# Optimization experiments

Hardware: AMD Instinct MI355X
Metric: run time of the kernel (lower is better)

Reference implementation:

```python
import jax, jax.numpy as jnp
import numpy as np

N = 10000          # nodes
E = 160000         # edges (avg degree 16)
H = 32             # hidden_dim
ND = 64            # node_dim
ED = 16            # edge_dim
MH = 128           # edge_mlp_hidden
MP_STEPS = 3


def setup_inputs() -> dict:
    key = jax.random.key(0)
    ks = jax.random.split(key, 10)
    s = lambda d: 1.0 / np.sqrt(d)
    return {
        "x": jax.random.normal(ks[0], (N, ND), jnp.float32),
        "edge_index": jax.random.randint(ks[1], (2, E), 0, N, dtype=jnp.int64),
        "edge_attr": jax.random.normal(ks[2], (E, ED), jnp.float32),
        # node_proj: Linear(node_dim -> hidden_dim)
        "Wp": jax.random.normal(ks[3], (ND, H), jnp.float32) * s(ND),
        "bp": jnp.zeros((H,), jnp.float32),
        # edge network MLP: edge_dim -> MH -> H*H
        "W1": jax.random.normal(ks[4], (ED, MH), jnp.float32) * s(ED),
        "b1": jnp.zeros((MH,), jnp.float32),
        "W2": jax.random.normal(ks[5], (MH, H * H), jnp.float32) * s(MH),
        "b2": jnp.zeros((H * H,), jnp.float32),
        # GRUCell params (torch layout: stacked [r, z, n], shape (3H, H))
        "w_ih": jax.random.normal(ks[6], (3 * H, H), jnp.float32) * s(H),
        "w_hh": jax.random.normal(ks[7], (3 * H, H), jnp.float32) * s(H),
        "b_ih": jnp.zeros((3 * H,), jnp.float32),
        "b_hh": jnp.zeros((3 * H,), jnp.float32),
    }


def gru_cell(x, h, w_ih, w_hh, b_ih, b_hh):
    # torch.nn.GRUCell semantics, gates stacked [r, z, n]
    gi = x @ w_ih.T + b_ih
    gh = h @ w_hh.T + b_hh
    i_r, i_z, i_n = jnp.split(gi, 3, axis=-1)
    h_r, h_z, h_n = jnp.split(gh, 3, axis=-1)
    r = jax.nn.sigmoid(i_r + h_r)
    z = jax.nn.sigmoid(i_z + h_z)
    n = jnp.tanh(i_n + r * h_n)
    return (1.0 - z) * n + z * h


def reference(x, edge_index, edge_attr, Wp, bp, W1, b1, W2, b2, w_ih, w_hh, b_ih, b_hh):
    h = x @ Wp + bp  # (N, H)
    # per-edge weight matrices; edge_attr is loop-invariant so compute once
    We = (jax.nn.relu(edge_attr @ W1 + b1) @ W2 + b2).reshape(E, H, H)
    src = edge_index[0]  # h_j (message source)
    dst = edge_index[1]  # aggregation target (PyG source_to_target flow)
    for _ in range(MP_STEPS):
        msg = jnp.einsum('eij,ej->ei', We, h[src])          # (E, H) per-edge GEMV
        agg = jax.ops.segment_sum(msg, dst, num_segments=N)  # scatter-add
        h = gru_cell(agg, h, w_ih, w_hh, b_ih, b_hh)
    return h
```

## Files before the change

### kernel.cpp

```cpp
#include <hip/hip_runtime.h>
#include <stdint.h>

#define H   32
#define ND  64
#define ED  16
#define MH  128
#define HH  1024

__device__ __forceinline__ float bf2f(uint16_t u) {
    union { uint32_t u; float f; } v; v.u = ((uint32_t)u) << 16; return v.f;
}
__device__ __forceinline__ uint16_t f2bf(float f) {
    union { float f; uint32_t u; } v; v.f = f;
    return (uint16_t)((v.u + 0x7FFFu + ((v.u >> 16) & 1u)) >> 16);
}
__device__ __forceinline__ float ldf(const void* p, size_t i, int isf32) {
    return isf32 ? ((const float*)p)[i] : bf2f(((const uint16_t*)p)[i]);
}

__global__ void k_detect(const uint16_t* __restrict__ xr,
                         const int* __restrict__ ei, int nedges,
                         int* __restrict__ flags) {
    __shared__ int s_bad, s_hi;
    int t = threadIdx.x;
    if (t == 0) { s_bad = 0; s_hi = 0; }
    __syncthreads();
    int bad = 0;
    for (int i = t; i < 2048; i += 256) {
        uint16_t u = xr[i];
        int e = (u >> 7) & 0xFF;
        if (!(u == 0 || (e >= 96 && e <= 144))) bad++;
    }
    atomicAdd(&s_bad, bad);
    int mm = nedges < 4096 ? nedges : 4096;
    int hi = 0;
    for (int i = t; i < mm; i += 256) hi |= (ei[2 * i + 1] != 0);
    if (hi) atomicOr(&s_hi, 1);
    __syncthreads();
    if (t == 0) {
        flags[0] = (s_bad > 204) ? 1 : 0;
        flags[1] = (s_hi == 0) ? 1 : 0;
    }
}

__device__ __forceinline__ int load_idx(const int* __restrict__ ei, int is64,
                                        long long pos, int nnodes) {
    int v = is64 ? (int)(((const long long*)ei)[pos]) : ei[pos];
    v = v < 0 ? 0 : v;
    return v >= nnodes ? nnodes - 1 : v;
}

__global__ void k_hist(const int* __restrict__ ei, const int* __restrict__ flags,
                       int* __restrict__ deg, int nedges, int nnodes) {
    int e = blockIdx.x * 256 + threadIdx.x;
    if (e >= nedges) return;
    int s = load_idx(ei, flags[1], e, nnodes);
    atomicAdd(&deg[s], 1);
}

__global__ void k_scan(const int* __restrict__ deg, int* __restrict__ cursor,
                       int nnodes) {
    __shared__ int tot[256];
    int t = threadIdx.x;
    int C = (nnodes + 255) >> 8;
    int b = t * C, e = b + C < nnodes ? b + C : nnodes;
    int s = 0;
    for (int i = b; i < e; i++) s += deg[i];
    tot[t] = s;
    __syncthreads();
    if (t == 0) {
        int acc = 0;
        for (int i = 0; i < 256; i++) { int v = tot[i]; tot[i] = acc; acc += v; }
    }
    __syncthreads();
    int acc = tot[t];
    for (int i = b; i < e; i++) { cursor[i] = acc; acc += deg[i]; }
}

__global__ void k_scatter(const int* __restrict__ ei, const int* __restrict__ flags,
                          int* __restrict__ cursor, int* __restrict__ perm,
                          int nedges, int nnodes) {
    int e = blockIdx.x * 256 + threadIdx.x;
    if (e >= nedges) return;
    int s = load_idx(ei, flags[1], e, nnodes);
    int p = atomicAdd(&cursor[s], 1);
    perm[p] = e;
}

__global__ __launch_bounds__(256) void k_node_proj(
    const void* __restrict__ x, const void* __restrict__ wp,
    const void* __restrict__ bp, float* __restrict__ h, int nnodes,
    const int* __restrict__ flags)
{
    __shared__ float wp_s[ND][H];
    __shared__ float x_s[8][ND + 1];
    int isf32 = flags[0];
    int t = threadIdx.x;
    for (int i = t; i < ND * H; i += 256) wp_s[i >> 5][i & 31] = ldf(wp, i, isf32);
    for (int i = t; i < 8 * ND; i += 256) {
        int row = i >> 6, col = i & 63;
        int gn = blockIdx.x * 8 + row;
        x_s[row][col] = (gn < nnodes) ? ldf(x, (size_t)gn * ND + col, isf32) : 0.f;
    }
    __syncthreads();
    int nl = t >> 5, c = t & 31;
    int n = blockIdx.x * 8 + nl;
    if (n >= nnodes) return;
    float acc = ldf(bp, c, isf32);
#pragma unroll
    for (int k = 0; k < ND; k++) acc += x_s[nl][k] * wp_s[k][c];
    h[(size_t)n * H + c] = acc;
}

__global__ void k_permw2(const void* __restrict__ w2g, float* __restrict__ Bp,
                         const int* __restrict__ flags) {
    int isf32 = flags[0];
    int idx = blockIdx.x * 256 + threadIdx.x;
    if (idx >= MH * HH) return;
    int k = idx / HH, col = idx % HH;
    int i = col >> 5, j = col & 31;
    Bp[(size_t)j * 4096 + i * 128 + k] = ldf(w2g, idx, isf32);
}

__global__ __launch_bounds__(256) void k_T4(
    const float* __restrict__ Bp, const float* __restrict__ h,
    float* __restrict__ Tall, int nnodes)
{
    __shared__ float h_s[64 * 32];
    int t = threadIdx.x;
    int cbq = blockIdx.x & 3;
    int n0 = (blockIdx.x >> 2) * 64;
    int c = cbq * 1024 + t * 4;

    for (int i = t; i < 64 * 32; i += 256) {
        int n = i >> 5;
        h_s[i] = (n0 + n < nnodes) ? h[(size_t)(n0 + n) * H + (i & 31)] : 0.f;
    }
    float4 Breg[32];
#pragma unroll
    for (int j = 0; j < 32; j++)
        Breg[j] = *((const float4*)&Bp[(size_t)j * 4096 + c]);
    __syncthreads();

    int nmax = nnodes - n0; if (nmax > 64) nmax = 64;
    int n = 0;
    for (; n + 2 <= nmax; n += 2) {
        float4 a0 = {0.f,0.f,0.f,0.f}, a1 = {0.f,0.f,0.f,0.f};
#pragma unroll
        for (int j = 0; j < 32; j++) {
            float h0 = h_s[n * 32 + j], h1 = h_s[(n + 1) * 32 + j];
            float4 b = Breg[j];
            a0.x += h0 * b.x; a0.y += h0 * b.y; a0.z += h0 * b.z; a0.w += h0 * b.w;
            a1.x += h1 * b.x; a1.y += h1 * b.y; a1.z += h1 * b.z; a1.w += h1 * b.w;
        }
        *((float4*)&Tall[(size_t)(n0 + n) * 4096 + c]) = a0;
        *((float4*)&Tall[(size_t)(n0 + n + 1) * 4096 + c]) = a1;
    }
    if (n < nmax) {
        float4 a0 = {0.f,0.f,0.f,0.f};
#pragma unroll
        for (int j = 0; j < 32; j++) {
            float h0 = h_s[n * 32 + j];
            float4 b = Breg[j];
            a0.x += h0 * b.x; a0.y += h0 * b.y; a0.z += h0 * b.z; a0.w += h0 * b.w;
        }
        *((float4*)&Tall[(size_t)(n0 + n) * 4096 + c]) = a0;
    }
}

__global__ __launch_bounds__(256) void k_u(
    const void* __restrict__ b2g, const float* __restrict__ h,
    float* __restrict__ u, int nnodes, const int* __restrict__ flags)
{
    __shared__ float b2_s[32 * 33];
    __shared__ float h_s[8 * 32];
    int isf32 = flags[0];
    int t = threadIdx.x;
    int n0 = blockIdx.x * 8;
    for (int idx = t; idx < 1024; idx += 256) {
        int i = idx >> 5, j = idx & 31;
        b2_s[i * 33 + j] = ldf(b2g, idx, isf32);
    }
    for (int i = t; i < 8 * 32; i += 256) {
        int n = i >> 5;
        h_s[i] = (n0 + n < nnodes) ? h[(size_t)(n0 + n) * H + (i & 31)] : 0.f;
    }
    __syncthreads();
    int nl = t >> 5, i = t & 31;
    if (n0 + nl >= nnodes) return;
    float acc = 0.f;
#pragma unroll
    for (int j = 0; j < 32; j++) acc += b2_s[i * 33 + j] * h_s[nl * 32 + j];
    u[(size_t)(n0 + nl) * 32 + i] = acc;
}

__global__ __launch_bounds__(256) void k_edge4(
    const void* __restrict__ ea, const void* __restrict__ w1,
    const void* __restrict__ b1g, const float* __restrict__ Tall,
    const float* __restrict__ u, const int* __restrict__ ei,
    const int* __restrict__ perm, const int* __restrict__ degp,
    const int* __restrict__ rendp, const int* __restrict__ flags,
    float* __restrict__ agg, int nedges, int nnodes)
{
    int n = blockIdx.x;
    int dcount = degp[n];
    if (dcount == 0) return;
    int rstart = rendp[n] - dcount;

    __shared__ float T_lds[32 * 132];
    __shared__ float hid_s[16 * 132];
    __shared__ float w1_s[ED * MH];
    __shared__ float ea_f[16 * ED];
    __shared__ float b1_s[MH];
    __shared__ float u_lds[32];
    __shared__ int   e_s[16], d_s[16];

    int t = threadIdx.x;
    int isf32 = flags[0], is64 = flags[1];

    for (int f = t; f < 1024; f += 256) {
        float4 q = *((const float4*)&Tall[(size_t)n * 4096 + f * 4]);
        int i = f >> 5, k4 = (f & 31) * 4;
        *((float4*)&T_lds[i * 132 + k4]) = q;
    }
    for (int i = t; i < ED * MH; i += 256) w1_s[i] = ldf(w1, i, isf32);
    if (t < MH) b1_s[t] = ldf(b1g, t, isf32);
    if (t < 32) u_lds[t] = u[(size_t)n * 32 + t];

    int e_rel = t & 15, i2 = t >> 4;
    int nchunks = (dcount + 15) >> 4;

    for (int ch = 0; ch < nchunks; ch++) {
        __syncthreads();
        if (t < 16) {
            int idx = ch * 16 + t;
            int e = (idx < dcount) ? perm[rstart + idx] : -1;
            e_s[t] = e;
            d_s[t] = (e >= 0) ? load_idx(ei, is64, (long long)nedges + e, nnodes) : 0;
        }
        __syncthreads();
        for (int i = t; i < 16 * ED; i += 256) {
            int e = e_s[i >> 4];
            ea_f[i] = (e >= 0) ? ldf(ea, (size_t)e * ED + (i & 15), isf32) : 0.f;
        }
        __syncthreads();
        for (int idx = t; idx < 16 * MH; idx += 256) {
            int el = idx >> 7, c = idx & 127;
            float acc = b1_s[c];
#pragma unroll
            for (int k = 0; k < ED; k++)
                acc += ea_f[el * ED + k] * w1_s[k * MH + c];
            hid_s[el * 132 + c] = fmaxf(acc, 0.f);
        }
        __syncthreads();
        if (e_s[e_rel] >= 0) {
            float a0 = u_lds[i2], a1 = u_lds[i2 + 16];
#pragma unroll
            for (int k4 = 0; k4 < 32; k4++) {
                float4 hv = *((const float4*)&hid_s[e_rel * 132 + k4 * 4]);
                float4 t0 = *((const float4*)&T_lds[i2 * 132 + k4 * 4]);
                float4 t1 = *((const float4*)&T_lds[(i2 + 16) * 132 + k4 * 4]);
                a0 += hv.x * t0.x + hv.y * t0.y + hv.z * t0.z + hv.w * t0.w;
                a1 += hv.x * t1.x + hv.y * t1.y + hv.z * t1.z + hv.w * t1.w;
            }
            int d = d_s[e_rel];
            atomicAdd(&agg[(size_t)d * H + i2], a0);
            atomicAdd(&agg[(size_t)d * H + i2 + 16], a1);
        }
    }
}

__global__ __launch_bounds__(256) void k_msg_valu(
    const void* __restrict__ ea, const void* __restrict__ w1,
    const void* __restrict__ b1g, const void* __restrict__ w2g,
    const void* __restrict__ b2g, const float* __restrict__ h,
    const int* __restrict__ ei, const int* __restrict__ flags,
    float* __restrict__ agg, int nedges, int nnodes)
{
    __shared__ float hid_s[64 * 130];
    __shared__ float w1_s[ED * MH];
    __shared__ float b1_s[MH];
    __shared__ float ea_f[64 * ED];

    int t = threadIdx.x;
    int e0 = blockIdx.x * 64;
    int isf32 = flags[0], is64 = flags[1];

    for (int i = t; i < 64 * ED; i += 256) {
        int e = e0 + (i >> 4);
        ea_f[i] = (e < nedges) ? ldf(ea, (size_t)e * ED + (i & 15), isf32) : 0.f;
    }
    for (int i = t; i < ED * MH; i += 256) w1_s[i] = ldf(w1, i, isf32);
    for (int i = t; i < MH; i += 256) b1_s[i] = ldf(b1g, i, isf32);
    __syncthreads();

    for (int idx = t; idx < 64 * MH; idx += 256) {
        int el = idx >> 7, c = idx & 127;
        float acc = b1_s[c];
#pragma unroll
        for (int k = 0; k < ED; k++)
            acc += ea_f[el * ED + k] * w1_s[k * MH + c];
        hid_s[el * 130 + c] = fmaxf(acc, 0.f);
    }
    __syncthreads();

    int lane = t & 63, w = t >> 6;
    int b = w * 64 + lane;
    int j = b & 31;
    int q = b >> 5;

    float b2v[4];
#pragma unroll
    for (int m = 0; m < 4; m++) b2v[m] = ldf(b2g, b + 256 * m, isf32);

    for (int g = 0; g < 4; g++) {
        float acc[16][4];
#pragma unroll
        for (int e = 0; e < 16; e++)
#pragma unroll
            for (int m = 0; m < 4; m++) acc[e][m] = 0.f;

        for (int k2 = 0; k2 < 64; k2++) {
            float w2a[4], w2b[4];
#pragma unroll
            for (int m = 0; m < 4; m++) {
                w2a[m] = ldf(w2g, (size_t)(2 * k2) * HH + b + 256 * m, isf32);
                w2b[m] = ldf(w2g, (size_t)(2 * k2 + 1) * HH + b + 256 * m, isf32);
            }
#pragma unroll
            for (int e = 0; e < 16; e++) {
                float2 hv = *((const float2*)&hid_s[(g * 16 + e) * 130 + 2 * k2]);
#pragma unroll
                for (int m = 0; m < 4; m++)
                    acc[e][m] += hv.x * w2a[m] + hv.y * w2b[m];
            }
        }

#pragma unroll
        for (int e = 0; e < 16; e++) {
            int eg = e0 + g * 16 + e;
            int valid = (eg < nedges);
            int se = valid ? load_idx(ei, is64, eg, nnodes) : 0;
            float he = h[(size_t)se * H + j];
            int d = valid ? load_idx(ei, is64, (long long)nedges + eg, nnodes) : 0;
#pragma unroll
            for (int m = 0; m < 4; m++) {
                float p = (acc[e][m] + b2v[m]) * he;
                p += __shfl_xor(p, 1);
                p += __shfl_xor(p, 2);
                p += __shfl_xor(p, 4);
                p += __shfl_xor(p, 8);
                p += __shfl_xor(p, 16);
                if ((lane & 31) == 0 && valid)
                    atomicAdd(&agg[(size_t)d * H + (q + 8 * m)], p);
            }
        }
    }
}

__global__ __launch_bounds__(256) void k_gru(
    const float* __restrict__ agg, const float* __restrict__ hin,
    const void* __restrict__ w_ih, const void* __restrict__ w_hh,
    const void* __restrict__ b_ih, const void* __restrict__ b_hh,
    float* __restrict__ hout, void* __restrict__ out_any,
    int nnodes, int finalstep, const int* __restrict__ flags)
{
    __shared__ float wih_s[3 * H][H + 1];
    __shared__ float whh_s[3 * H][H + 1];
    __shared__ float bih_s[3 * H], bhh_s[3 * H];
    __shared__ float a_s[8][H + 1], h_s[8][H + 1];
    int isf32 = flags[0];
    int t = threadIdx.x;
    for (int i = t; i < 3 * H * H; i += 256) {
        wih_s[i >> 5][i & 31] = ldf(w_ih, i, isf32);
        whh_s[i >> 5][i & 31] = ldf(w_hh, i, isf32);
    }
    for (int i = t; i < 3 * H; i += 256) {
        bih_s[i] = ldf(b_ih, i, isf32);
        bhh_s[i] = ldf(b_hh, i, isf32);
    }
    int nl = t >> 5, i = t & 31;
    int n = blockIdx.x * 8 + nl;
    if (n < nnodes) {
        a_s[nl][i] = agg[(size_t)n * H + i];
        h_s[nl][i] = hin[(size_t)n * H + i];
    }
    __syncthreads();
    if (n >= nnodes) return;

    float gr = bih_s[i], gz = bih_s[H + i], gn = bih_s[2 * H + i];
    float hr = bhh_s[i], hz = bhh_s[H + i], hn = bhh_s[2 * H + i];
#pragma unroll
    for (int jj = 0; jj < H; jj++) {
        float a = a_s[nl][jj], hh = h_s[nl][jj];
        gr += a * wih_s[i][jj];      gz += a * wih_s[H + i][jj];  gn += a * wih_s[2 * H + i][jj];
        hr += hh * whh_s[i][jj];     hz += hh * whh_s[H + i][jj]; hn += hh * whh_s[2 * H + i][jj];
    }
    float r  = 1.f / (1.f + __expf(-(gr + hr)));
    float z  = 1.f / (1.f + __expf(-(gz + hz)));
    float nv = tanhf(gn + r * hn);
    float hnew = (1.f - z) * nv + z * h_s[nl][i];
    hout[(size_t)n * H + i] = hnew;
    if (finalstep) {
        if (isf32) ((float*)out_any)[(size_t)n * H + i] = hnew;
        else       ((uint16_t*)out_any)[(size_t)n * H + i] = f2bf(hnew);
    }
}

extern "C" void kernel_launch(void* const* d_in, const int* in_sizes, int n_in,
                              void* d_out, int out_size, void* d_ws, size_t ws_size,
                              hipStream_t stream)
{
    const void* x   = d_in[0];
    const int*  ei  = (const int*)d_in[1];
    const void* ea  = d_in[2];
    const void* wp  = d_in[3];
    const void* bp  = d_in[4];
    const void* w1  = d_in[5];
    const void* b1  = d_in[6];
    const void* w2  = d_in[7];
    const void* b2  = d_in[8];
    const void* wih = d_in[9];
    const void* whh = d_in[10];
    const void* bih = d_in[11];
    const void* bhh = d_in[12];

    int nnodes = in_sizes[0] / ND;
    int nedges = in_sizes[1] / 2;

    size_t hbytes = (size_t)nnodes * H * sizeof(float);
    size_t tbytes = (size_t)nnodes * 4096 * sizeof(float);
    if (ws_size < 256 + 2 * hbytes) return;

    size_t off = 0;
    int*   flags  = (int*)d_ws;                 off += 256;
    float* bufA   = (float*)((char*)d_ws + off); off += hbytes;
    float* bufB   = (float*)((char*)d_ws + off); off += hbytes;
    float* u_buf  = (float*)((char*)d_ws + off); off += hbytes;
    int*   deg    = (int*)((char*)d_ws + off);   off += (size_t)nnodes * 4;
    int*   cursor = (int*)((char*)d_ws + off);   off += (size_t)nnodes * 4;
    int*   perm   = (int*)((char*)d_ws + off);   off += (size_t)nedges * 4;
    off = (off + 255) & ~(size_t)255;
    float* Bperm  = (float*)((char*)d_ws + off); off += (size_t)MH * HH * 4;
    off = (off + 255) & ~(size_t)255;
    float* Tall   = (float*)((char*)d_ws + off); off += tbytes;
    int hi_tier = (ws_size >= off);

    k_detect<<<1, 256, 0, stream>>>((const uint16_t*)x, ei, nedges, flags);
    k_node_proj<<<(nnodes + 7) / 8, 256, 0, stream>>>(x, wp, bp, bufA, nnodes, flags);

    if (hi_tier) {
        hipMemsetAsync(deg, 0, (size_t)nnodes * 4, stream);
        k_hist<<<(nedges + 255) / 256, 256, 0, stream>>>(ei, flags, deg, nedges, nnodes);
        k_scan<<<1, 256, 0, stream>>>(deg, cursor, nnodes);
        k_scatter<<<(nedges + 255) / 256, 256, 0, stream>>>(ei, flags, cursor, perm, nedges, nnodes);
        k_permw2<<<(MH * HH + 255) / 256, 256, 0, stream>>>(w2, Bperm, flags);
    }

    float* hcur = bufA;
    float* aggb = bufB;
    for (int s = 0; s < 3; s++) {
        hipMemsetAsync(aggb, 0, hbytes, stream);
        if (hi_tier) {
            k_T4<<<((nnodes + 63) / 64) * 4, 256, 0, stream>>>(
                Bperm, hcur, Tall, nnodes);
            k_u<<<(nnodes + 7) / 8, 256, 0, stream>>>(b2, hcur, u_buf, nnodes, flags);
            k_edge4<<<nnodes, 256, 0, stream>>>(
                ea, w1, b1, Tall, u_buf, ei, perm, deg, cursor, flags,
                aggb, nedges, nnodes);
        } else {
            k_msg_valu<<<(nedges + 63) / 64, 256, 0, stream>>>(
                ea, w1, b1, w2, b2, hcur, ei, flags, aggb, nedges, nnodes);
        }
        k_gru<<<(nnodes + 7) / 8, 256, 0, stream>>>(
            aggb, hcur, wih, whh, bih, bhh, aggb, d_out, nnodes, s == 2, flags);
        float* tmp = hcur; hcur = aggb; aggb = tmp;
    }
}
```

Before: 862.0 us.

## Fuse bias GEMV into T kernel, fold agg zeroing into GRU, streamline edge kernel

The per-node b2·h product (u) is now computed inside k_T4 by the first column-block, which removes the separate k_u launch. The h tile in k_T4 is padded to a row stride of 33 to avoid LDS bank conflicts. The per-step agg memset is replaced by having k_gru zero the old h buffer after reading it, with one initial memset before the loop. In the edge kernel, all 256 threads load edge attributes in parallel, one sync per chunk is dropped, and the hidden layer is vectorised with float4. The cost is redundant per-thread perm and edge-index loads in place of the shared-memory broadcast.

```diff
diff --git a/kernel.cpp b/kernel.cpp
--- a/kernel.cpp
+++ b/kernel.cpp
@@ -123,18 +123,19 @@
 }
 
 __global__ __launch_bounds__(256) void k_T4(
-    const float* __restrict__ Bp, const float* __restrict__ h,
-    float* __restrict__ Tall, int nnodes)
-{
-    __shared__ float h_s[64 * 32];
+    const float* __restrict__ Bp, const void* __restrict__ b2g,
+    const float* __restrict__ h, float* __restrict__ Tall,
+    float* __restrict__ u, int nnodes, const int* __restrict__ flags)
+{
+    __shared__ float h_s[64 * 33];
     int t = threadIdx.x;
     int cbq = blockIdx.x & 3;
     int n0 = (blockIdx.x >> 2) * 64;
     int c = cbq * 1024 + t * 4;
 
     for (int i = t; i < 64 * 32; i += 256) {
-        int n = i >> 5;
-        h_s[i] = (n0 + n < nnodes) ? h[(size_t)(n0 + n) * H + (i & 31)] : 0.f;
+        int n = i >> 5, j = i & 31;
+        h_s[n * 33 + j] = (n0 + n < nnodes) ? h[(size_t)(n0 + n) * H + j] : 0.f;
     }
     float4 Breg[32];
 #pragma unroll
@@ -148,7 +149,7 @@
         float4 a0 = {0.f,0.f,0.f,0.f}, a1 = {0.f,0.f,0.f,0.f};
 #pragma unroll
         for (int j = 0; j < 32; j++) {
-            float h0 = h_s[n * 32 + j], h1 = h_s[(n + 1) * 32 + j];
+            float h0 = h_s[n * 33 + j], h1 = h_s[(n + 1) * 33 + j];
             float4 b = Breg[j];
             a0.x += h0 * b.x; a0.y += h0 * b.y; a0.z += h0 * b.z; a0.w += h0 * b.w;
             a1.x += h1 * b.x; a1.y += h1 * b.y; a1.z += h1 * b.z; a1.w += h1 * b.w;
@@ -160,41 +161,35 @@
         float4 a0 = {0.f,0.f,0.f,0.f};
 #pragma unroll
         for (int j = 0; j < 32; j++) {
-            float h0 = h_s[n * 32 + j];
+            float h0 = h_s[n * 33 + j];
             float4 b = Breg[j];
             a0.x += h0 * b.x; a0.y += h0 * b.y; a0.z += h0 * b.z; a0.w += h0 * b.w;
         }
         *((float4*)&Tall[(size_t)(n0 + n) * 4096 + c]) = a0;
     }
-}
-
-__global__ __launch_bounds__(256) void k_u(
-    const void* __restrict__ b2g, const float* __restrict__ h,
-    float* __restrict__ u, int nnodes, const int* __restrict__ flags)
-{
-    __shared__ float b2_s[32 * 33];
-    __shared__ float h_s[8 * 32];
-    int isf32 = flags[0];
-    int t = threadIdx.x;
-    int n0 = blockIdx.x * 8;
-    for (int idx = t; idx < 1024; idx += 256) {
-        int i = idx >> 5, j = idx & 31;
-        b2_s[i * 33 + j] = ldf(b2g, idx, isf32);
-    }
-    for (int i = t; i < 8 * 32; i += 256) {
-        int n = i >> 5;
-        h_s[i] = (n0 + n < nnodes) ? h[(size_t)(n0 + n) * H + (i & 31)] : 0.f;
-    }
-    __syncthreads();
-    int nl = t >> 5, i = t & 31;
-    if (n0 + nl >= nnodes) return;
-    float acc = 0.f;
-#pragma unroll
-    for (int j = 0; j < 32; j++) acc += b2_s[i * 33 + j] * h_s[nl * 32 + j];
-    u[(size_t)(n0 + nl) * 32 + i] = acc;
-}
-
-__global__ __launch_bounds__(256) void k_edge4(
+
+    if (cbq == 0) {
+        int isf32 = flags[0];
+        int nl = t >> 2, iq = (t & 3) * 8;
+        if (n0 + nl < nnodes) {
+            float acc[8];
+#pragma unroll
+            for (int m = 0; m < 8; m++) acc[m] = 0.f;
+#pragma unroll
+            for (int j = 0; j < 32; j++) {
+                float hv = h_s[nl * 33 + j];
+#pragma unroll
+                for (int m = 0; m < 8; m++)
+                    acc[m] += ldf(b2g, (iq + m) * 32 + j, isf32) * hv;
+            }
+#pragma unroll
+            for (int m = 0; m < 8; m++)
+                u[(size_t)(n0 + nl) * 32 + iq + m] = acc[m];
+        }
+    }
+}
+
+__global__ __launch_bounds__(256) void k_edge5(
     const void* __restrict__ ea, const void* __restrict__ w1,
     const void* __restrict__ b1g, const float* __restrict__ Tall,
     const float* __restrict__ u, const int* __restrict__ ei,
@@ -213,7 +208,6 @@
     __shared__ float ea_f[16 * ED];
     __shared__ float b1_s[MH];
     __shared__ float u_lds[32];
-    __shared__ int   e_s[16], d_s[16];
 
     int t = threadIdx.x;
     int isf32 = flags[0], is64 = flags[1];
@@ -232,28 +226,33 @@
 
     for (int ch = 0; ch < nchunks; ch++) {
         __syncthreads();
-        if (t < 16) {
-            int idx = ch * 16 + t;
+        {
+            int slot = t >> 4, kk = t & 15;
+            int idx = ch * 16 + slot;
             int e = (idx < dcount) ? perm[rstart + idx] : -1;
-            e_s[t] = e;
-            d_s[t] = (e >= 0) ? load_idx(ei, is64, (long long)nedges + e, nnodes) : 0;
+            ea_f[slot * ED + kk] = (e >= 0) ? ldf(ea, (size_t)e * ED + kk, isf32)
+                                            : 0.f;
         }
         __syncthreads();
-        for (int i = t; i < 16 * ED; i += 256) {
-            int e = e_s[i >> 4];
-            ea_f[i] = (e >= 0) ? ldf(ea, (size_t)e * ED + (i & 15), isf32) : 0.f;
+        for (int idx = t; idx < 512; idx += 256) {
+            int el = idx >> 5, c4 = (idx & 31) * 4;
+            float4 a = *((const float4*)&b1_s[c4]);
+#pragma unroll
+            for (int k = 0; k < ED; k++) {
+                float ev = ea_f[el * ED + k];
+                float4 wv = *((const float4*)&w1_s[k * MH + c4]);
+                a.x += ev * wv.x; a.y += ev * wv.y;
+                a.z += ev * wv.z; a.w += ev * wv.w;
+            }
+            a.x = fmaxf(a.x, 0.f); a.y = fmaxf(a.y, 0.f);
+            a.z = fmaxf(a.z, 0.f); a.w = fmaxf(a.w, 0.f);
+            *((float4*)&hid_s[el * 132 + c4]) = a;
         }
         __syncthreads();
-        for (int idx = t; idx < 16 * MH; idx += 256) {
-            int el = idx >> 7, c = idx & 127;
-            float acc = b1_s[c];
-#pragma unroll
-            for (int k = 0; k < ED; k++)
-                acc += ea_f[el * ED + k] * w1_s[k * MH + c];
-            hid_s[el * 132 + c] = fmaxf(acc, 0.f);
-        }
-        __syncthreads();
-        if (e_s[e_rel] >= 0) {
+        int idx = ch * 16 + e_rel;
+        if (idx < dcount) {
+            int e = perm[rstart + idx];
+            int d = load_idx(ei, is64, (long long)nedges + e, nnodes);
             float a0 = u_lds[i2], a1 = u_lds[i2 + 16];
 #pragma unroll
             for (int k4 = 0; k4 < 32; k4++) {
@@ -263,7 +262,6 @@
                 a0 += hv.x * t0.x + hv.y * t0.y + hv.z * t0.z + hv.w * t0.w;
                 a1 += hv.x * t1.x + hv.y * t1.y + hv.z * t1.z + hv.w * t1.w;
             }
-            int d = d_s[e_rel];
             atomicAdd(&agg[(size_t)d * H + i2], a0);
             atomicAdd(&agg[(size_t)d * H + i2 + 16], a1);
         }
@@ -359,7 +357,7 @@
 }
 
 __global__ __launch_bounds__(256) void k_gru(
-    const float* __restrict__ agg, const float* __restrict__ hin,
+    const float* __restrict__ agg, float* hin,
     const void* __restrict__ w_ih, const void* __restrict__ w_hh,
     const void* __restrict__ b_ih, const void* __restrict__ b_hh,
     float* __restrict__ hout, void* __restrict__ out_any,
@@ -401,6 +399,7 @@
     float nv = tanhf(gn + r * hn);
     float hnew = (1.f - z) * nv + z * h_s[nl][i];
     hout[(size_t)n * H + i] = hnew;
+    hin[(size_t)n * H + i] = 0.f;
     if (finalstep) {
         if (isf32) ((float*)out_any)[(size_t)n * H + i] = hnew;
         else       ((uint16_t*)out_any)[(size_t)n * H + i] = f2bf(hnew);
@@ -448,6 +447,7 @@
 
     k_detect<<<1, 256, 0, stream>>>((const uint16_t*)x, ei, nedges, flags);
     k_node_proj<<<(nnodes + 7) / 8, 256, 0, stream>>>(x, wp, bp, bufA, nnodes, flags);
+    hipMemsetAsync(bufB, 0, hbytes, stream);
 
     if (hi_tier) {
         hipMemsetAsync(deg, 0, (size_t)nnodes * 4, stream);
@@ -460,12 +460,10 @@
     float* hcur = bufA;
     float* aggb = bufB;
     for (int s = 0; s < 3; s++) {
-        hipMemsetAsync(aggb, 0, hbytes, stream);
         if (hi_tier) {
             k_T4<<<((nnodes + 63) / 64) * 4, 256, 0, stream>>>(
-                Bperm, hcur, Tall, nnodes);
-            k_u<<<(nnodes + 7) / 8, 256, 0, stream>>>(b2, hcur, u_buf, nnodes, flags);
-            k_edge4<<<nnodes, 256, 0, stream>>>(
+                Bperm, b2, hcur, Tall, u_buf, nnodes, flags);
+            k_edge5<<<nnodes, 256, 0, stream>>>(
                 ea, w1, b1, Tall, u_buf, ei, perm, deg, cursor, flags,
                 aggb, nedges, nnodes);
         } else {
```

Result: slower. 1.094 ms (+26.9%).
